# Kernel tuning notes

Measured on AMD Instinct MI355X. Metric: run time of the kernel, lower is better.

The kernel has to match this reference:

```python
import jax, jax.numpy as jnp
import numpy as np

NUM_ELEC = 128
TIME_STEPS = 128  # must equal NUM_ELEC for the original module's matmuls to be shape-consistent
NUM_VOXELS = 2052
HIDDEN = 64
DCT_DIM = 512
BATCH = 64
RHO = 0.5
TAU = 0.1
PLV_THRESH = 0.5


def dct_matrix(N, K):
    n = np.arange(N)[None, :]
    k = np.arange(K)[:, None]
    m = np.sqrt(2.0 / N) * np.cos(np.pi * (2 * n + 1) * k / (2 * N))
    m[0, :] = 1.0 / np.sqrt(N)
    return jnp.asarray(m, dtype=jnp.float32)


def setup_inputs() -> dict:
    ks = jax.random.split(jax.random.key(0), 12)
    H = HIDDEN
    return {
        "z": jax.random.normal(ks[0], (BATCH, NUM_ELEC, TIME_STEPS), dtype=jnp.float32),
        "lead_field": jax.random.normal(ks[1], (NUM_VOXELS, NUM_ELEC), dtype=jnp.float32),
        "gumbel_u": jax.random.uniform(ks[2], (NUM_ELEC, NUM_ELEC), dtype=jnp.float32, minval=1e-6, maxval=1.0 - 1e-6),
        "w_gae": jax.random.normal(ks[3], (NUM_ELEC, H), dtype=jnp.float32) / np.sqrt(NUM_ELEC),
        "b_gae": jnp.zeros((H,), dtype=jnp.float32),
        "w1": jax.random.normal(ks[4], (NUM_ELEC, H), dtype=jnp.float32) / np.sqrt(NUM_ELEC),
        "b1": jnp.zeros((H,), dtype=jnp.float32),
        "w2": jax.random.normal(ks[5], (H, H), dtype=jnp.float32) / np.sqrt(H),
        "b2": jnp.zeros((H,), dtype=jnp.float32),
        "w_ih": jax.random.normal(ks[6], (3 * H, H), dtype=jnp.float32) / np.sqrt(H),
        "w_hh": jax.random.normal(ks[7], (3 * H, H), dtype=jnp.float32) / np.sqrt(H),
        "b_ih": jnp.zeros((3 * H,), dtype=jnp.float32),
        "b_hh": jnp.zeros((3 * H,), dtype=jnp.float32),
    }


def _hilbert_phases(z):
    # FFT-based analytic signal along last axis (== scipy.signal.hilbert), then instantaneous phase
    T = z.shape[-1]
    idx = jnp.arange(T)
    hf = jnp.where(idx == 0, 1.0, jnp.where(idx < T // 2, 2.0, jnp.where(idx == T // 2, 1.0, 0.0)))
    analytic = jnp.fft.ifft(jnp.fft.fft(z, axis=-1) * hf, axis=-1)
    return jnp.angle(analytic)


def _forward(z, lead_field, gumbel_u, w_gae, b_gae, w1, b1, w2, b2, w_ih, w_hh, b_ih, b_hh):
    B, N, T = z.shape
    # ---- PLV adjacency: fused broadcast+reduction replacing the 128x128 python double loop ----
    phases = _hilbert_phases(z)                                  # [B,N,T]
    E = jnp.exp(1j * phases).astype(jnp.complex64)
    # plv[i,j] = |mean_{b,t} exp(i(phi_i - phi_j))| = |E_i . conj(E_j)| / (B*T)
    plv = jnp.abs(jnp.einsum('bit,bjt->ij', E, jnp.conj(E))) / (B * T)
    a = (plv >= PLV_THRESH).astype(jnp.float32)                  # [N,N]
    # ---- GAE: GCN encoder on batch-averaged signals + inner-product decoder ----
    x = jnp.mean(z, axis=0)                                      # [N,T] (T == N)
    hg = jax.nn.relu((a @ x) @ w_gae + b_gae)                    # [N,H]
    p = jax.nn.sigmoid(hg @ hg.T)                                # [N,N]
    # ---- Gumbel graph augmentation ----
    e = RHO * p + (1.0 - RHO) * a
    g = -jnp.log(-jnp.log(gumbel_u))
    a_aug = jax.nn.sigmoid((jnp.log(e) - jnp.log(1.0 - e) + g) / TAU)
    # ---- symmetric degree normalization ----
    d_inv_sqrt = jnp.sum(a_aug, axis=-1) ** -0.5
    a_norm = d_inv_sqrt[:, None] * a_aug * d_inv_sqrt[None, :]
    zT = jnp.swapaxes(z, 1, 2)                                   # [B,T,N]
    h = jax.nn.relu(jnp.matmul(a_norm, zT) @ w1 + b1)            # [B,N,H]
    h = jax.nn.relu(jnp.matmul(a_norm, h) @ w2 + b2)             # [B,N,H]
    h_seq = h.reshape(B * T, -1)                                 # [B*T,H]
    # ---- GRU over flattened (B*T) sequence (torch nn.GRU gate order r,z,n) ----
    Hd = w_hh.shape[1]
    def gru_step(hprev, xt):
        gi = xt @ w_ih.T + b_ih
        gh = hprev @ w_hh.T + b_hh
        ir, iz, inn = jnp.split(gi, 3)
        hr, hz, hn = jnp.split(gh, 3)
        r = jax.nn.sigmoid(ir + hr)
        zg = jax.nn.sigmoid(iz + hz)
        cand = jnp.tanh(inn + r * hn)
        hnew = (1.0 - zg) * cand + zg * hprev
        return hnew, hnew
    _, h_gru = jax.lax.scan(gru_step, jnp.zeros((Hd,), z.dtype), h_seq)
    del h_gru  # computed as in the original forward, but not part of the returned tuple
    # ---- lead-field projection + DCT low-pass reconstruction ----
    dct_m = dct_matrix(NUM_VOXELS, DCT_DIM)                      # [K,V]
    s = jnp.matmul(lead_field, zT)                               # [B,V,T]
    s_dct = jnp.matmul(dct_m, s)                                 # [B,K,T]
    s_low = s_dct[:, :DCT_DIM, :]                                # [B,K,T] (full, K == dct_dim)
    s_recon = jnp.matmul(dct_m.T, s_low)                         # [B,V,T]
    return s_low, s_recon, a_aug


def reference(z, lead_field, gumbel_u, w_gae, b_gae, w1, b1, w2, b2, w_ih, w_hh, b_ih, b_hh):
    return _forward(z, lead_field, gumbel_u, w_gae, b_gae, w1, b1, w2, b2, w_ih, w_hh, b_ih, b_hh)
```

## Files before the change

### kernel.cpp

```cpp
#include <hip/hip_runtime.h>

#define NV 2052
#define KD 512
#define RTOT 2564
#define KTOT 256
#define JTOT 8192

typedef __attribute__((ext_vector_type(8))) short short8v;
typedef __attribute__((ext_vector_type(4))) float f32x4;
typedef unsigned short ushort_t;

#define OFF_AF   0u
#define OFF_ABF  65536u
#define OFF_BBF  409600u
#define OFF_YBF  1458176u
#define OFF_PG   2506752u
#define OFF_PM1  6701056u
#define OFF_A    7749632u
#define OFF_X    7766016u
#define OFF_XW   7782400u

#define SREC_OFF 4194304u
#define AAUG_OFF 21004288u

#define GLOAD16(g, l) __builtin_amdgcn_global_load_lds( \
    (const __attribute__((address_space(1))) unsigned int*)(g), \
    (__attribute__((address_space(3))) unsigned int*)(l), 16, 0, 0)

__device__ __forceinline__ float dct_val(int k, int v) {
    if (k == 0) return 1.0f / sqrtf(2052.0f);
    int m = (2 * v + 1) * k;
    int r = m % 8208;
    float ang = (float)((double)r * (3.14159265358979323846 / 4104.0));
    return sqrtf(2.0f / 2052.0f) * cosf(ang);
}

__device__ __forceinline__ void bf16split(float x, ushort_t& hi, ushort_t& lo) {
    unsigned xb = __float_as_uint(x);
    hi = (ushort_t)(xb >> 16);
    float r = x - __uint_as_float((unsigned)hi << 16);
    lo = (ushort_t)(__float_as_uint(r) >> 16);
}

__device__ __forceinline__ ushort_t bf16rn(float x) {
    unsigned xb = __float_as_uint(x);
    return (ushort_t)((xb + 0x7fffu + ((xb >> 16) & 1u)) >> 16);
}

__global__ __launch_bounds__(256) void k_front(const float* __restrict__ LF, const float* __restrict__ z,
                                               float* __restrict__ Pm1,
                                               ushort_t* __restrict__ Ybf, ushort_t* __restrict__ Bbf) {
    __shared__ float sh[8][132];
    const int tid = threadIdx.x;
    const int bid = blockIdx.x;
    if (bid < 1024) {
        const int t = tid & 127;
        const int kk = tid >> 7;
        const int k0 = (bid & 63) * 8;
        const int vch = bid >> 6;
        const int v0 = vch * 128;
        const int nv = (vch == 15) ? 132 : 128;
        for (int p = tid; p < 1056; p += 256) {
            int rr = p / 132, cc = p - rr * 132;
            sh[rr][cc] = dct_val(k0 + rr, v0 + cc);
        }
        __syncthreads();
        const float* lf = LF + (size_t)v0 * 128 + t;
        float a0 = 0.f, a1 = 0.f, a2 = 0.f, a3 = 0.f;
        for (int vi = 0; vi + 2 <= nv; vi += 2) {
            float l0 = lf[vi * 128], l1 = lf[vi * 128 + 128];
            a0 += sh[kk + 0][vi] * l0; a1 += sh[kk + 2][vi] * l0;
            a2 += sh[kk + 4][vi] * l0; a3 += sh[kk + 6][vi] * l0;
            a0 += sh[kk + 0][vi + 1] * l1; a1 += sh[kk + 2][vi + 1] * l1;
            a2 += sh[kk + 4][vi + 1] * l1; a3 += sh[kk + 6][vi + 1] * l1;
        }
        float* P = Pm1 + (size_t)vch * 65536;
        P[(k0 + kk + 0) * 128 + t] = a0;
        P[(k0 + kk + 2) * 128 + t] = a1;
        P[(k0 + kk + 4) * 128 + t] = a2;
        P[(k0 + kk + 6) * 128 + t] = a3;
    } else {
        const int t = tid & 127;
        const int rr = tid >> 7;
        const int rid = (bid - 1024) * 2 + rr;
        const int b = rid >> 7, i = rid & 127;
        sh[rr][t] = z[(size_t)rid * 128 + t];
        if (tid < 128) {
            float hv = 0.f;
            if (t & 1) {
                float ang = 3.14159265358979323846f * (float)t * (1.0f / 128.0f);
                hv = (cosf(ang) / sinf(ang)) * (1.0f / 64.0f);
            }
            sh[2][t] = hv;
        }
        __syncthreads();
        float acc = 0.f;
        #pragma unroll 8
        for (int q = 0; q < 64; ++q) {
            int d = 2 * q + 1;
            acc += sh[2][d] * sh[rr][(t - d) & 127];
        }
        float zv = sh[rr][t];
        float inv = rsqrtf(zv * zv + acc * acc);
        Ybf[(size_t)i * JTOT + b * 128 + t] = bf16rn(zv * inv);
        Ybf[(size_t)(128 + i) * JTOT + b * 128 + t] = bf16rn(acc * inv);
        ushort_t hi = (ushort_t)(__float_as_uint(zv) >> 16);
        ushort_t* row = Bbf + (size_t)rid * KTOT;
        row[t] = hi; row[128 + t] = hi;
    }
}

__global__ __launch_bounds__(256) void k_m1red(const float* __restrict__ Pm1, const float* __restrict__ z,
                                               float* __restrict__ AF, ushort_t* __restrict__ Abf,
                                               float* __restrict__ X) {
    const int bid = blockIdx.x;
    if (bid < 256) {
        int id = bid * 256 + threadIdx.x;
        float s = 0.f;
        #pragma unroll
        for (int p = 0; p < 16; ++p) s += Pm1[p * 65536 + id];
        AF[id] = s;
        int rid = id >> 7, t = id & 127;
        ushort_t hi, lo; bf16split(s, hi, lo);
        ushort_t* row = Abf + (size_t)rid * KTOT;
        row[t] = hi; row[128 + t] = lo;
    } else {
        int id = (bid - 256) * 256 + threadIdx.x;
        float s0 = 0.f, s1 = 0.f, s2 = 0.f, s3 = 0.f;
        #pragma unroll 4
        for (int b = 0; b < 64; b += 4) {
            s0 += z[(size_t)(b + 0) * 16384 + id];
            s1 += z[(size_t)(b + 1) * 16384 + id];
            s2 += z[(size_t)(b + 2) * 16384 + id];
            s3 += z[(size_t)(b + 3) * 16384 + id];
        }
        X[id] = ((s0 + s1) + (s2 + s3)) * (1.0f / 64.0f);
    }
}

__global__ __launch_bounds__(256) void k_m2(const float* __restrict__ M1, ushort_t* __restrict__ Abf) {
    __shared__ float sM1[128][128];
    __shared__ float sdct[8][128];
    const int tid = threadIdx.x;
    const int t = tid & 127;
    const int half = tid >> 7;
    const int v0 = blockIdx.x * 8;
    float acc0 = 0.f, acc1 = 0.f, acc2 = 0.f, acc3 = 0.f;
    for (int kc = 0; kc < KD; kc += 128) {
        __syncthreads();
        #pragma unroll
        for (int q = 0; q < 16; ++q) {
            int f = q * 256 + tid;
            int kr = f >> 5;
            int c4 = (f & 31) * 4;
            *(float4*)&sM1[kr][c4] = *(const float4*)&M1[(size_t)(kc + kr) * 128 + c4];
        }
        #pragma unroll
        for (int p = tid; p < 1024; p += 256)
            sdct[p >> 7][p & 127] = dct_val(kc + (p & 127), v0 + (p >> 7));
        __syncthreads();
        const float* d0 = &sdct[half * 4 + 0][0];
        const float* d1 = &sdct[half * 4 + 1][0];
        const float* d2 = &sdct[half * 4 + 2][0];
        const float* d3 = &sdct[half * 4 + 3][0];
        #pragma unroll 4
        for (int ki = 0; ki < 128; ++ki) {
            float m = sM1[ki][t];
            acc0 += d0[ki] * m;
            acc1 += d1[ki] * m;
            acc2 += d2[ki] * m;
            acc3 += d3[ki] * m;
        }
    }
    float vals[4] = {acc0, acc1, acc2, acc3};
    #pragma unroll
    for (int r = 0; r < 4; ++r) {
        int v = v0 + half * 4 + r;
        if (v < NV) {
            ushort_t hi, lo; bf16split(vals[r], hi, lo);
            ushort_t* row = Abf + (size_t)(KD + v) * KTOT;
            row[t] = hi; row[128 + t] = lo;
        }
    }
}

__global__ __launch_bounds__(256) void k_back(const ushort_t* __restrict__ Abf, const ushort_t* __restrict__ Bbf,
                                              const ushort_t* __restrict__ Ybf,
                                              float* __restrict__ out, float* __restrict__ Pg) {
    __shared__ float SMf[8704];
    ushort_t* Al = (ushort_t*)SMf;
    ushort_t* Bl = Al + 8192;
    const int tid = threadIdx.x;
    const int wave = tid >> 6;
    const int lane = tid & 63;
    const int wr = wave >> 1, wc = wave & 1;
    const int l15 = lane & 15;
    const int lhi = lane >> 4;
    const int bid = blockIdx.x;

    f32x4 acc[4][4];
    #pragma unroll
    for (int i = 0; i < 4; ++i)
        #pragma unroll
        for (int j = 0; j < 4; ++j)
            acc[i][j] = (f32x4){0.f, 0.f, 0.f, 0.f};

    if (bid < 1344) {
        const int j0 = (bid & 63) * 128;
        const int r0 = (bid >> 6) * 128;
        for (int kc = 0; kc < KTOT; kc += 64) {
            __syncthreads();
            #pragma unroll
            for (int i = 0; i < 4; ++i) {
                int elt = (wave * 4 + i) * 64 + lane;
                int m = elt >> 3;
                int sc = (elt & 7) ^ (m & 7);
                GLOAD16(Abf + (size_t)(r0 + m) * KTOT + kc + sc * 8, &Al[(wave * 4 + i) * 512]);
                GLOAD16(Bbf + (size_t)(j0 + m) * KTOT + kc + sc * 8, &Bl[(wave * 4 + i) * 512]);
            }
            asm volatile("s_waitcnt vmcnt(0)" ::: "memory");
            __syncthreads();
            #pragma unroll
            for (int kk = 0; kk < 2; ++kk) {
                short8v av[4], bv[4];
                #pragma unroll
                for (int mi = 0; mi < 4; ++mi) {
                    int m = wr * 64 + mi * 16 + l15;
                    int ch = (kk * 4 + lhi) ^ (m & 7);
                    av[mi] = *(const short8v*)&Al[m * 64 + ch * 8];
                }
                #pragma unroll
                for (int ni = 0; ni < 4; ++ni) {
                    int n = wc * 64 + ni * 16 + l15;
                    int ch = (kk * 4 + lhi) ^ (n & 7);
                    bv[ni] = *(const short8v*)&Bl[n * 64 + ch * 8];
                }
                #pragma unroll
                for (int mi = 0; mi < 4; ++mi)
                    #pragma unroll
                    for (int ni = 0; ni < 4; ++ni)
                        acc[mi][ni] = __builtin_amdgcn_mfma_f32_16x16x32_bf16(av[mi], bv[ni], acc[mi][ni], 0, 0, 0);
            }
        }
        const unsigned bb = (unsigned)(bid & 63);
        #pragma unroll
        for (int hhalf = 0; hhalf < 2; ++hhalf) {
            __syncthreads();
            if (wc == hhalf) {
                #pragma unroll
                for (int mi = 0; mi < 4; ++mi)
                    #pragma unroll
                    for (int ni = 0; ni < 4; ++ni)
                        #pragma unroll
                        for (int reg = 0; reg < 4; ++reg) {
                            int rl = wr * 64 + mi * 16 + lhi * 4 + reg;
                            int cl = ni * 16 + l15;
                            SMf[rl * 68 + cl] = acc[mi][ni][reg];
                        }
            }
            __syncthreads();
            int rl = tid >> 1;
            int cs = (tid & 1) * 32;
            int r = r0 + rl;
            if (r < RTOT) {
                unsigned base;
                if (r < KD) base = bb * 65536u + (unsigned)r * 128u;
                else        base = SREC_OFF + bb * 262656u + (unsigned)(r - KD) * 128u;
                base += hhalf * 64 + cs;
                const float* src = &SMf[rl * 68 + cs];
                float* dst = out + base;
                #pragma unroll
                for (int q = 0; q < 8; ++q)
                    *(float4*)(dst + q * 4) = *(const float4*)(src + q * 4);
            }
        }
    } else {
        const int g = bid - 1344;
        const int j0 = (g & 1) * 128;
        const int i0 = ((g >> 1) & 1) * 128;
        const int sk = g >> 2;
        const int kc0 = sk * 128;
        for (int kc = kc0; kc < kc0 + 128; kc += 64) {
            __syncthreads();
            #pragma unroll
            for (int i = 0; i < 4; ++i) {
                int elt = (wave * 4 + i) * 64 + lane;
                int m = elt >> 3;
                int sc = (elt & 7) ^ (m & 7);
                GLOAD16(Ybf + (size_t)(i0 + m) * JTOT + kc + sc * 8, &Al[(wave * 4 + i) * 512]);
                GLOAD16(Ybf + (size_t)(j0 + m) * JTOT + kc + sc * 8, &Bl[(wave * 4 + i) * 512]);
            }
            asm volatile("s_waitcnt vmcnt(0)" ::: "memory");
            __syncthreads();
            #pragma unroll
            for (int kk = 0; kk < 2; ++kk) {
                short8v av[4], bv[4];
                #pragma unroll
                for (int mi = 0; mi < 4; ++mi) {
                    int m = wr * 64 + mi * 16 + l15;
                    int ch = (kk * 4 + lhi) ^ (m & 7);
                    av[mi] = *(const short8v*)&Al[m * 64 + ch * 8];
                }
                #pragma unroll
                for (int ni = 0; ni < 4; ++ni) {
                    int n = wc * 64 + ni * 16 + l15;
                    int ch = (kk * 4 + lhi) ^ (n & 7);
                    bv[ni] = *(const short8v*)&Bl[n * 64 + ch * 8];
                }
                #pragma unroll
                for (int mi = 0; mi < 4; ++mi)
                    #pragma unroll
                    for (int ni = 0; ni < 4; ++ni)
                        acc[mi][ni] = __builtin_amdgcn_mfma_f32_16x16x32_bf16(av[mi], bv[ni], acc[mi][ni], 0, 0, 0);
            }
        }
        const int q = ((g >> 1) & 1) * 2 + (g & 1);
        float* P = Pg + (size_t)(sk * 4 + q) * 16384;
        #pragma unroll
        for (int mi = 0; mi < 4; ++mi)
            #pragma unroll
            for (int reg = 0; reg < 4; ++reg) {
                int rl = wr * 64 + mi * 16 + lhi * 4 + reg;
                #pragma unroll
                for (int ni = 0; ni < 4; ++ni) {
                    int cl = wc * 64 + ni * 16 + l15;
                    P[rl * 128 + cl] = acc[mi][ni][reg];
                }
            }
    }
}

__global__ __launch_bounds__(256) void k_plvx(const float* __restrict__ Pg, const float* __restrict__ X,
                                              const float* __restrict__ Wg,
                                              float* __restrict__ A, float* __restrict__ XW) {
    const int bid = blockIdx.x;
    if (bid < 64) {
        int id = bid * 256 + threadIdx.x;
        float R = 0.f, I = 0.f;
        #pragma unroll 8
        for (int sk = 0; sk < 64; ++sk) {
            const float* P = Pg + (size_t)sk * 65536 + id;
            R += P[0] + P[3 * 16384];
            I += P[2 * 16384] - P[1 * 16384];
        }
        float plv = sqrtf(R * R + I * I) * (1.0f / 8192.0f);
        A[id] = (plv >= 0.5f) ? 1.0f : 0.0f;
    } else {
        int id = (bid - 64) * 256 + threadIdx.x;
        int e = id >> 6, h = id & 63;
        const float* xrow = X + (size_t)e * 128;
        float s = 0.f;
        #pragma unroll 4
        for (int t = 0; t < 128; ++t) s += xrow[t] * Wg[t * 64 + h];
        XW[id] = s;
    }
}

__global__ __launch_bounds__(256) void k_aaugf(const float* __restrict__ A, const float* __restrict__ XW,
                                               const float* __restrict__ bg, const float* __restrict__ U,
                                               float* __restrict__ out) {
    __shared__ float sXW[128][64];
    __shared__ float sHGT[64][128];
    const int tid = threadIdx.x;
    for (int p = tid; p < 8192; p += 256) sXW[p >> 6][p & 63] = XW[p];
    __syncthreads();
    {
        const int r = tid & 127;
        const int half = tid >> 7;
        const float* arow = A + (size_t)r * 128;
        float hacc[32];
        #pragma unroll
        for (int h = 0; h < 32; ++h) hacc[h] = 0.f;
        for (int j = 0; j < 128; ++j) {
            float av = arow[j];
            #pragma unroll
            for (int h = 0; h < 32; ++h) hacc[h] += av * sXW[j][half * 32 + h];
        }
        #pragma unroll
        for (int h = 0; h < 32; ++h)
            sHGT[half * 32 + h][r] = fmaxf(hacc[h] + bg[half * 32 + h], 0.f);
    }
    __syncthreads();
    const int id = blockIdx.x * 256 + tid;
    const int i = id >> 7, j = id & 127;
    float dot = 0.f;
    #pragma unroll 8
    for (int h = 0; h < 64; ++h) dot += sHGT[h][i] * sHGT[h][j];
    float p = 1.f / (1.f + expf(-dot));
    float e = 0.5f * p + 0.5f * A[id];
    float gmb = -logf(-logf(U[id]));
    float arg = (logf(e) - logf(1.f - e) + gmb) * 10.0f;
    out[AAUG_OFF + id] = 1.f / (1.f + expf(-arg));
}

extern "C" void kernel_launch(void* const* d_in, const int* in_sizes, int n_in,
                              void* d_out, int out_size, void* d_ws, size_t ws_size,
                              hipStream_t stream) {
    const float* z  = (const float*)d_in[0];
    const float* LF = (const float*)d_in[1];
    const float* U  = (const float*)d_in[2];
    const float* Wg = (const float*)d_in[3];
    const float* bg = (const float*)d_in[4];
    float* out = (float*)d_out;
    float* W = (float*)d_ws;

    float* AF  = W + OFF_AF;
    ushort_t* Abf = (ushort_t*)(W + OFF_ABF);
    ushort_t* Bbf = (ushort_t*)(W + OFF_BBF);
    ushort_t* Ybf = (ushort_t*)(W + OFF_YBF);
    float* Pg  = W + OFF_PG;
    float* Pm1 = W + OFF_PM1;
    float* A   = W + OFF_A;
    float* X   = W + OFF_X;
    float* XW  = W + OFF_XW;

    k_front<<<5120, 256, 0, stream>>>(LF, z, Pm1, Ybf, Bbf);
    k_m1red<<<320, 256, 0, stream>>>(Pm1, z, AF, Abf, X);
    k_m2   <<<257, 256, 0, stream>>>(AF, Abf);
    k_back <<<1600, 256, 0, stream>>>(Abf, Bbf, Ybf, out, Pg);
    k_plvx <<<96, 256, 0, stream>>>(Pg, X, Wg, A, XW);
    k_aaugf<<<64, 256, 0, stream>>>(A, XW, bg, U, out);
}
```

Baseline: 115.1 us.

## Share B tile between hi/lo A halves and halve PLV split-K blocks

The split-bf16 GEMM used to store B duplicated as [hi,hi] across a K of 256. It now stores B once with K of 128, and for each B fragment loads the A hi and lo parts and issues two MFMAs. This removes the duplicate B global loads and the B workspace writes, at the cost of a larger LDS footprint (48KB instead of about 34KB), which may lower occupancy. The PLV split-K also moves from 64 to 32 chunks, each 256 deep, so there are fewer blocks and less partial-sum traffic, and the reduction loop is adjusted to match.

```diff
diff --git a/kernel.cpp b/kernel.cpp
--- a/kernel.cpp
+++ b/kernel.cpp
@@ -104,9 +104,7 @@
         float inv = rsqrtf(zv * zv + acc * acc);
         Ybf[(size_t)i * JTOT + b * 128 + t] = bf16rn(zv * inv);
         Ybf[(size_t)(128 + i) * JTOT + b * 128 + t] = bf16rn(acc * inv);
-        ushort_t hi = (ushort_t)(__float_as_uint(zv) >> 16);
-        ushort_t* row = Bbf + (size_t)rid * KTOT;
-        row[t] = hi; row[128 + t] = hi;
+        Bbf[(size_t)rid * 128 + t] = (ushort_t)(__float_as_uint(zv) >> 16);
     }
 }
 
@@ -187,9 +185,7 @@
 __global__ __launch_bounds__(256) void k_back(const ushort_t* __restrict__ Abf, const ushort_t* __restrict__ Bbf,
                                               const ushort_t* __restrict__ Ybf,
                                               float* __restrict__ out, float* __restrict__ Pg) {
-    __shared__ float SMf[8704];
-    ushort_t* Al = (ushort_t*)SMf;
-    ushort_t* Bl = Al + 8192;
+    __shared__ ushort_t SM[24576];
     const int tid = threadIdx.x;
     const int wave = tid >> 6;
     const int lane = tid & 63;
@@ -208,26 +204,31 @@
     if (bid < 1344) {
         const int j0 = (bid & 63) * 128;
         const int r0 = (bid >> 6) * 128;
-        for (int kc = 0; kc < KTOT; kc += 64) {
+        ushort_t* AlHi = SM;
+        ushort_t* AlLo = SM + 8192;
+        ushort_t* Bl   = SM + 16384;
+        for (int kc = 0; kc < 128; kc += 64) {
             __syncthreads();
             #pragma unroll
             for (int i = 0; i < 4; ++i) {
                 int elt = (wave * 4 + i) * 64 + lane;
                 int m = elt >> 3;
                 int sc = (elt & 7) ^ (m & 7);
-                GLOAD16(Abf + (size_t)(r0 + m) * KTOT + kc + sc * 8, &Al[(wave * 4 + i) * 512]);
-                GLOAD16(Bbf + (size_t)(j0 + m) * KTOT + kc + sc * 8, &Bl[(wave * 4 + i) * 512]);
+                GLOAD16(Abf + (size_t)(r0 + m) * KTOT + kc + sc * 8,       &AlHi[(wave * 4 + i) * 512]);
+                GLOAD16(Abf + (size_t)(r0 + m) * KTOT + 128 + kc + sc * 8, &AlLo[(wave * 4 + i) * 512]);
+                GLOAD16(Bbf + (size_t)(j0 + m) * 128 + kc + sc * 8,        &Bl[(wave * 4 + i) * 512]);
             }
             asm volatile("s_waitcnt vmcnt(0)" ::: "memory");
             __syncthreads();
             #pragma unroll
             for (int kk = 0; kk < 2; ++kk) {
-                short8v av[4], bv[4];
+                short8v ah[4], al[4], bv[4];
                 #pragma unroll
                 for (int mi = 0; mi < 4; ++mi) {
                     int m = wr * 64 + mi * 16 + l15;
                     int ch = (kk * 4 + lhi) ^ (m & 7);
-                    av[mi] = *(const short8v*)&Al[m * 64 + ch * 8];
+                    ah[mi] = *(const short8v*)&AlHi[m * 64 + ch * 8];
+                    al[mi] = *(const short8v*)&AlLo[m * 64 + ch * 8];
                 }
                 #pragma unroll
                 for (int ni = 0; ni < 4; ++ni) {
@@ -239,9 +240,15 @@
                 for (int mi = 0; mi < 4; ++mi)
                     #pragma unroll
                     for (int ni = 0; ni < 4; ++ni)
-                        acc[mi][ni] = __builtin_amdgcn_mfma_f32_16x16x32_bf16(av[mi], bv[ni], acc[mi][ni], 0, 0, 0);
-            }
-        }
+                        acc[mi][ni] = __builtin_amdgcn_mfma_f32_16x16x32_bf16(ah[mi], bv[ni], acc[mi][ni], 0, 0, 0);
+                #pragma unroll
+                for (int mi = 0; mi < 4; ++mi)
+                    #pragma unroll
+                    for (int ni = 0; ni < 4; ++ni)
+                        acc[mi][ni] = __builtin_amdgcn_mfma_f32_16x16x32_bf16(al[mi], bv[ni], acc[mi][ni], 0, 0, 0);
+            }
+        }
+        float* SMf = (float*)SM;
         const unsigned bb = (unsigned)(bid & 63);
         #pragma unroll
         for (int hhalf = 0; hhalf < 2; ++hhalf) {
@@ -279,8 +286,10 @@
         const int j0 = (g & 1) * 128;
         const int i0 = ((g >> 1) & 1) * 128;
         const int sk = g >> 2;
-        const int kc0 = sk * 128;
-        for (int kc = kc0; kc < kc0 + 128; kc += 64) {
+        const int kc0 = sk * 256;
+        ushort_t* Al = SM;
+        ushort_t* Bl = SM + 8192;
+        for (int kc = kc0; kc < kc0 + 256; kc += 64) {
             __syncthreads();
             #pragma unroll
             for (int i = 0; i < 4; ++i) {
@@ -338,7 +347,7 @@
         int id = bid * 256 + threadIdx.x;
         float R = 0.f, I = 0.f;
         #pragma unroll 8
-        for (int sk = 0; sk < 64; ++sk) {
+        for (int sk = 0; sk < 32; ++sk) {
             const float* P = Pg + (size_t)sk * 65536 + id;
             R += P[0] + P[3 * 16384];
             I += P[2 * 16384] - P[1 * 16384];
@@ -417,7 +426,7 @@
     k_front<<<5120, 256, 0, stream>>>(LF, z, Pm1, Ybf, Bbf);
     k_m1red<<<320, 256, 0, stream>>>(Pm1, z, AF, Abf, X);
     k_m2   <<<257, 256, 0, stream>>>(AF, Abf);
-    k_back <<<1600, 256, 0, stream>>>(Abf, Bbf, Ybf, out, Pg);
+    k_back <<<1472, 256, 0, stream>>>(Abf, Bbf, Ybf, out, Pg);
     k_plvx <<<96, 256, 0, stream>>>(Pg, X, Wg, A, XW);
     k_aaugf<<<64, 256, 0, stream>>>(A, XW, bg, U, out);
 }
```

New measurement: 112.8 us. About the same (-2.0%).
